# Kernel optimization log

Hardware: AMD Instinct MI355X
Metric: run time of the kernel (lower is better)

## Reference

```python
import jax, jax.numpy as jnp
import numpy as np

N, C = 16384, 512

def setup_inputs() -> dict:
    key = jax.random.key(0)
    k1, k2 = jax.random.split(key)
    mean = jax.random.normal(k1, (N, C), dtype=jnp.float32)
    var = jax.random.uniform(k2, (N, C), dtype=jnp.float32)  # positive diagonal variances
    return {"mean": mean, "var": var, "num_samples": 400}

def reference(mean, var, num_samples):
    # Monte Carlo estimate of E[softmax(mean + eps)], eps ~ N(0, diag(var)).
    # lax.scan keeps memory flat (no [S, N, C] buffer), matching the torch loop.
    std = jnp.sqrt(var)
    keys = jax.random.split(jax.random.key(42), num_samples)

    def body(acc, k):
        eps = jax.random.normal(k, mean.shape, dtype=mean.dtype) * std
        return acc + jax.nn.softmax(mean + eps, axis=-1), None

    acc, _ = jax.lax.scan(body, jnp.zeros_like(mean), keys)
    return acc / num_samples
```

## Files before the change

### kernel.cpp

```cpp
#include <hip/hip_runtime.h>
#include <stdint.h>

static __device__ __forceinline__ uint32_t rotl32(uint32_t v, int n) {
  return (v << n) | (v >> (32 - n));
}

static __device__ __forceinline__ void threefry2x32(
    uint32_t k0, uint32_t k1, uint32_t x0, uint32_t x1,
    uint32_t& o0, uint32_t& o1)
{
  const uint32_t ks2 = k0 ^ k1 ^ 0x1BD11BDAu;
  x0 += k0; x1 += k1;

  x0 += x1; x1 = rotl32(x1, 13); x1 ^= x0;
  x0 += x1; x1 = rotl32(x1, 15); x1 ^= x0;
  x0 += x1; x1 = rotl32(x1, 26); x1 ^= x0;
  x0 += x1; x1 = rotl32(x1,  6); x1 ^= x0;
  x0 += k1; x1 += ks2 + 1u;

  x0 += x1; x1 = rotl32(x1, 17); x1 ^= x0;
  x0 += x1; x1 = rotl32(x1, 29); x1 ^= x0;
  x0 += x1; x1 = rotl32(x1, 16); x1 ^= x0;
  x0 += x1; x1 = rotl32(x1, 24); x1 ^= x0;
  x0 += ks2; x1 += k0 + 2u;

  x0 += x1; x1 = rotl32(x1, 13); x1 ^= x0;
  x0 += x1; x1 = rotl32(x1, 15); x1 ^= x0;
  x0 += x1; x1 = rotl32(x1, 26); x1 ^= x0;
  x0 += x1; x1 = rotl32(x1,  6); x1 ^= x0;
  x0 += k0; x1 += k1 + 3u;

  x0 += x1; x1 = rotl32(x1, 17); x1 ^= x0;
  x0 += x1; x1 = rotl32(x1, 29); x1 ^= x0;
  x0 += x1; x1 = rotl32(x1, 16); x1 ^= x0;
  x0 += x1; x1 = rotl32(x1, 24); x1 ^= x0;
  x0 += k1; x1 += ks2 + 4u;

  x0 += x1; x1 = rotl32(x1, 13); x1 ^= x0;
  x0 += x1; x1 = rotl32(x1, 15); x1 ^= x0;
  x0 += x1; x1 = rotl32(x1, 26); x1 ^= x0;
  x0 += x1; x1 = rotl32(x1,  6); x1 ^= x0;
  x0 += ks2; x1 += k0 + 5u;

  o0 = x0; o1 = x1;
}

static __device__ __forceinline__ float erfinv_f(float x) {
  float t = fmaf(x, -x, 1.0f);
  float w = -__logf(t);
  float p;
  if (w < 5.0f) {
    w = w - 2.5f;
    p =              2.81022636e-08f;
    p = fmaf(p, w,   3.43273939e-07f);
    p = fmaf(p, w,  -3.5233877e-06f);
    p = fmaf(p, w,  -4.39150654e-06f);
    p = fmaf(p, w,   0.00021858087f);
    p = fmaf(p, w,  -0.00125372503f);
    p = fmaf(p, w,  -0.00417768164f);
    p = fmaf(p, w,   0.246640727f);
    p = fmaf(p, w,   1.50140941f);
  } else {
    w = __builtin_amdgcn_sqrtf(w) - 3.0f;
    p =             -0.000200214257f;
    p = fmaf(p, w,   0.000100950558f);
    p = fmaf(p, w,   0.00134934322f);
    p = fmaf(p, w,  -0.00367342844f);
    p = fmaf(p, w,   0.00573950773f);
    p = fmaf(p, w,  -0.0076224613f);
    p = fmaf(p, w,   0.00943887047f);
    p = fmaf(p, w,   1.00167406f);
    p = fmaf(p, w,   2.83297682f);
  }
  return p * x;
}

#define NSAMP 400
#define NC 512

__global__ __launch_bounds__(256, 4) void mc_softmax_kernel(
    const float* __restrict__ mean, const float* __restrict__ var,
    float* __restrict__ out)
{
  __shared__ uint2 kb[NSAMP];
  for (int s = threadIdx.x; s < NSAMP; s += 256) {
    uint32_t a, b;
    threefry2x32(0u, 42u, 0u, (uint32_t)s, a, b);
    kb[s] = make_uint2(a, b);
  }
  __syncthreads();

  const int lane  = threadIdx.x & 63;
  const int row   = (blockIdx.x << 2) + (threadIdx.x >> 6);
  const int cbase = lane << 2;

  const float* mr = mean + (size_t)row * NC;
  const float* vr = var  + (size_t)row * NC;

  float m[8], sd[8], acc[8], e[8];
  {
    float4 t0 = *(const float4*)(mr + cbase);
    float4 t1 = *(const float4*)(mr + 256 + cbase);
    m[0] = t0.x; m[1] = t0.y; m[2] = t0.z; m[3] = t0.w;
    m[4] = t1.x; m[5] = t1.y; m[6] = t1.z; m[7] = t1.w;
    float4 v0 = *(const float4*)(vr + cbase);
    float4 v1 = *(const float4*)(vr + 256 + cbase);
    sd[0] = sqrtf(v0.x); sd[1] = sqrtf(v0.y); sd[2] = sqrtf(v0.z); sd[3] = sqrtf(v0.w);
    sd[4] = sqrtf(v1.x); sd[5] = sqrtf(v1.y); sd[6] = sqrtf(v1.z); sd[7] = sqrtf(v1.w);
  }
#pragma unroll
  for (int j = 0; j < 8; ++j) acc[j] = 0.0f;

  const uint32_t base = (uint32_t)(row * NC + cbase);
  const float lo = -0.99999994f;
  const float sqrt2 = 1.41421356237f;

  for (int s = 0; s < NSAMP; ++s) {
    const uint2 kk = kb[s];
    const uint32_t k0 = kk.x;
    const uint32_t k1 = kk.y;
    float sum = 0.0f;
#pragma unroll
    for (int j = 0; j < 8; ++j) {
      const uint32_t cnt = base + (uint32_t)(j < 4 ? j : 252 + j);
      uint32_t y0, y1;
      threefry2x32(k0, k1, 0u, cnt, y0, y1);
      const uint32_t bits = y0 ^ y1;
      float f = __uint_as_float((bits >> 9) | 0x3f800000u) - 1.0f;
      float u = fmaf(f, 2.0f, lo);
      float nrm = sqrt2 * erfinv_f(u);
      float lg  = fmaf(nrm, sd[j], m[j]);
      float ex  = __expf(lg);
      e[j] = ex;
      sum += ex;
    }
#pragma unroll
    for (int off = 32; off >= 1; off >>= 1)
      sum += __shfl_xor(sum, off);
    const float inv = __builtin_amdgcn_rcpf(sum);
#pragma unroll
    for (int j = 0; j < 8; ++j)
      acc[j] = fmaf(e[j], inv, acc[j]);
  }

  float* orow = out + (size_t)row * NC;
  const float sc = 1.0f / (float)NSAMP;
  float4 o0, o1;
  o0.x = acc[0] * sc; o0.y = acc[1] * sc; o0.z = acc[2] * sc; o0.w = acc[3] * sc;
  o1.x = acc[4] * sc; o1.y = acc[5] * sc; o1.z = acc[6] * sc; o1.w = acc[7] * sc;
  *(float4*)(orow + cbase)       = o0;
  *(float4*)(orow + 256 + cbase) = o1;
}

extern "C" void kernel_launch(void* const* d_in, const int* in_sizes, int n_in,
                              void* d_out, int out_size, void* d_ws, size_t ws_size,
                              hipStream_t stream) {
  const float* mean = (const float*)d_in[0];
  const float* var  = (const float*)d_in[1];
  float* out        = (float*)d_out;

  const int rows = out_size / NC;
  const int blocks = rows / 4;
  mc_softmax_kernel<<<blocks, 256, 0, stream>>>(mean, var, out);
}
```

Measured before the change: 7.101 ms.

## Process two samples per iteration, fold constants into exp2/log2, compute keys inline

Unrolls the sample loop by two so the two threefry streams and the two wave reductions interleave, giving more independent work for latency hiding. Folds sqrt2 and log2(e) into precomputed per-element scale and offset so the inner loop uses raw exp2/log2 builtins with fewer multiplies. Replaces the shared-memory key table and its barrier with keys recomputed inline, and swaps the mantissa shift/or for an alignbit. Two samples in flight raise register pressure, and the recomputed keys add threefry work per sample pair.

```diff
diff --git a/kernel.cpp b/kernel.cpp
--- a/kernel.cpp
+++ b/kernel.cpp
@@ -1,5 +1,19 @@
 #include <hip/hip_runtime.h>
 #include <stdint.h>
+
+#define NSAMP 400
+#define NC 512
+
+#if __has_builtin(__builtin_amdgcn_exp2f)
+#define EXP2F(x) __builtin_amdgcn_exp2f(x)
+#else
+#define EXP2F(x) __expf((x) * 0.6931471805599453f)
+#endif
+#if __has_builtin(__builtin_amdgcn_logf)
+#define LOG2F(x) __builtin_amdgcn_logf(x)
+#else
+#define LOG2F(x) (__logf(x) * 1.4426950408889634f)
+#endif
 
 static __device__ __forceinline__ uint32_t rotl32(uint32_t v, int n) {
   return (v << n) | (v >> (32 - n));
@@ -45,12 +59,16 @@
   o0 = x0; o1 = x1;
 }
 
-static __device__ __forceinline__ float erfinv_f(float x) {
-  float t = fmaf(x, -x, 1.0f);
-  float w = -__logf(t);
+static __device__ __forceinline__ uint32_t tf_bits(uint32_t k0, uint32_t k1, uint32_t cnt) {
+  uint32_t y0, y1;
+  threefry2x32(k0, k1, 0u, cnt, y0, y1);
+  return y0 ^ y1;
+}
+
+static __device__ __forceinline__ float softexp(float u, float L, float sd2, float m2) {
   float p;
-  if (w < 5.0f) {
-    w = w - 2.5f;
+  if (L > -7.2134752f) {
+    float w = fmaf(L, -0.69314718f, -2.5f);
     p =              2.81022636e-08f;
     p = fmaf(p, w,   3.43273939e-07f);
     p = fmaf(p, w,  -3.5233877e-06f);
@@ -61,7 +79,7 @@
     p = fmaf(p, w,   0.246640727f);
     p = fmaf(p, w,   1.50140941f);
   } else {
-    w = __builtin_amdgcn_sqrtf(w) - 3.0f;
+    float w = __builtin_amdgcn_sqrtf(L * -0.69314718f) - 3.0f;
     p =             -0.000200214257f;
     p = fmaf(p, w,   0.000100950558f);
     p = fmaf(p, w,   0.00134934322f);
@@ -72,24 +90,16 @@
     p = fmaf(p, w,   1.00167406f);
     p = fmaf(p, w,   2.83297682f);
   }
-  return p * x;
+  float px = p * u;
+  return EXP2F(fmaf(px, sd2, m2));
 }
 
-#define NSAMP 400
-#define NC 512
-
-__global__ __launch_bounds__(256, 4) void mc_softmax_kernel(
-    const float* __restrict__ mean, const float* __restrict__ var,
-    float* __restrict__ out)
+__global__ __launch_bounds__(256)
+__attribute__((amdgpu_waves_per_eu(4, 4)))
+void mc_softmax_kernel(const float* __restrict__ mean,
+                       const float* __restrict__ var,
+                       float* __restrict__ out)
 {
-  __shared__ uint2 kb[NSAMP];
-  for (int s = threadIdx.x; s < NSAMP; s += 256) {
-    uint32_t a, b;
-    threefry2x32(0u, 42u, 0u, (uint32_t)s, a, b);
-    kb[s] = make_uint2(a, b);
-  }
-  __syncthreads();
-
   const int lane  = threadIdx.x & 63;
   const int row   = (blockIdx.x << 2) + (threadIdx.x >> 6);
   const int cbase = lane << 2;
@@ -97,50 +107,73 @@
   const float* mr = mean + (size_t)row * NC;
   const float* vr = var  + (size_t)row * NC;
 
-  float m[8], sd[8], acc[8], e[8];
+  float m2[8], sd2[8], acc[8];
   {
+    const float L2E = 1.4426950408889634f;
+    const float S2L = 2.0402788959f;
     float4 t0 = *(const float4*)(mr + cbase);
     float4 t1 = *(const float4*)(mr + 256 + cbase);
-    m[0] = t0.x; m[1] = t0.y; m[2] = t0.z; m[3] = t0.w;
-    m[4] = t1.x; m[5] = t1.y; m[6] = t1.z; m[7] = t1.w;
+    m2[0] = t0.x * L2E; m2[1] = t0.y * L2E; m2[2] = t0.z * L2E; m2[3] = t0.w * L2E;
+    m2[4] = t1.x * L2E; m2[5] = t1.y * L2E; m2[6] = t1.z * L2E; m2[7] = t1.w * L2E;
     float4 v0 = *(const float4*)(vr + cbase);
     float4 v1 = *(const float4*)(vr + 256 + cbase);
-    sd[0] = sqrtf(v0.x); sd[1] = sqrtf(v0.y); sd[2] = sqrtf(v0.z); sd[3] = sqrtf(v0.w);
-    sd[4] = sqrtf(v1.x); sd[5] = sqrtf(v1.y); sd[6] = sqrtf(v1.z); sd[7] = sqrtf(v1.w);
+    sd2[0] = __builtin_amdgcn_sqrtf(v0.x) * S2L;
+    sd2[1] = __builtin_amdgcn_sqrtf(v0.y) * S2L;
+    sd2[2] = __builtin_amdgcn_sqrtf(v0.z) * S2L;
+    sd2[3] = __builtin_amdgcn_sqrtf(v0.w) * S2L;
+    sd2[4] = __builtin_amdgcn_sqrtf(v1.x) * S2L;
+    sd2[5] = __builtin_amdgcn_sqrtf(v1.y) * S2L;
+    sd2[6] = __builtin_amdgcn_sqrtf(v1.z) * S2L;
+    sd2[7] = __builtin_amdgcn_sqrtf(v1.w) * S2L;
   }
 #pragma unroll
   for (int j = 0; j < 8; ++j) acc[j] = 0.0f;
 
   const uint32_t base = (uint32_t)(row * NC + cbase);
   const float lo = -0.99999994f;
-  const float sqrt2 = 1.41421356237f;
 
-  for (int s = 0; s < NSAMP; ++s) {
-    const uint2 kk = kb[s];
-    const uint32_t k0 = kk.x;
-    const uint32_t k1 = kk.y;
-    float sum = 0.0f;
+  for (int s = 0; s < NSAMP; s += 2) {
+    uint32_t a0, a1, b0, b1;
+    threefry2x32(0u, 42u, 0u, (uint32_t)s,       a0, a1);
+    threefry2x32(0u, 42u, 0u, (uint32_t)(s + 1), b0, b1);
+
+    float uA[8], LA[8], uB[8], LB[8];
 #pragma unroll
     for (int j = 0; j < 8; ++j) {
       const uint32_t cnt = base + (uint32_t)(j < 4 ? j : 252 + j);
-      uint32_t y0, y1;
-      threefry2x32(k0, k1, 0u, cnt, y0, y1);
-      const uint32_t bits = y0 ^ y1;
-      float f = __uint_as_float((bits >> 9) | 0x3f800000u) - 1.0f;
-      float u = fmaf(f, 2.0f, lo);
-      float nrm = sqrt2 * erfinv_f(u);
-      float lg  = fmaf(nrm, sd[j], m[j]);
-      float ex  = __expf(lg);
-      e[j] = ex;
-      sum += ex;
+      {
+        uint32_t bits = tf_bits(a0, a1, cnt);
+        float f = __uint_as_float(__builtin_amdgcn_alignbit(0x7Fu, bits, 9u)) - 1.0f;
+        float u = fmaf(f, 2.0f, lo);
+        uA[j] = u;
+        LA[j] = LOG2F(fmaf(u, -u, 1.0f));
+      }
+      {
+        uint32_t bits = tf_bits(b0, b1, cnt);
+        float f = __uint_as_float(__builtin_amdgcn_alignbit(0x7Fu, bits, 9u)) - 1.0f;
+        float u = fmaf(f, 2.0f, lo);
+        uB[j] = u;
+        LB[j] = LOG2F(fmaf(u, -u, 1.0f));
+      }
     }
+
+    float eA[8], eB[8], sumA = 0.0f, sumB = 0.0f;
 #pragma unroll
-    for (int off = 32; off >= 1; off >>= 1)
-      sum += __shfl_xor(sum, off);
-    const float inv = __builtin_amdgcn_rcpf(sum);
+    for (int j = 0; j < 8; ++j) {
+      eA[j] = softexp(uA[j], LA[j], sd2[j], m2[j]); sumA += eA[j];
+      eB[j] = softexp(uB[j], LB[j], sd2[j], m2[j]); sumB += eB[j];
+    }
+
+#pragma unroll
+    for (int off = 32; off >= 1; off >>= 1) {
+      sumA += __shfl_xor(sumA, off);
+      sumB += __shfl_xor(sumB, off);
+    }
+    const float invA = __builtin_amdgcn_rcpf(sumA);
+    const float invB = __builtin_amdgcn_rcpf(sumB);
 #pragma unroll
     for (int j = 0; j < 8; ++j)
-      acc[j] = fmaf(e[j], inv, acc[j]);
+      acc[j] = fmaf(eA[j], invA, fmaf(eB[j], invB, acc[j]));
   }
 
   float* orow = out + (size_t)row * NC;
```

New measurement: 7.260 ms. 1.02x slower.
